# Performance work log

Hardware: AMD Instinct MI355X
Metric: run time of the kernel (lower is better)

Reference implementation:

```python
import jax, jax.numpy as jnp
import numpy as np
from jax import lax

K = 3            # kernel_size
PAD = (K - 1) // 2


def zero_insert_stride2(x):
    # tf_pad_with_stride for stride=2, f_conv!=1, padding='SAME':
    # interleave a zero BEFORE each element along W then H -> [b, 2h, 2w, c]
    b, h, w, c = x.shape
    z1 = jnp.zeros_like(x)
    med1 = jnp.stack([z1, x], axis=3).reshape(b, h, 2 * w, c)
    z2 = jnp.zeros_like(med1)
    return jnp.stack([z2, med1], axis=2).reshape(b, 2 * h, 2 * w, c)


def conv_valid(x, w):
    return lax.conv_general_dilated(
        x, w, window_strides=(1, 1), padding='VALID',
        dimension_numbers=('NHWC', 'HWIO', 'NHWC'))


def backward_conv(grad_output, inputs, kernels):
    p = PAD
    # --- grad w.r.t. input: zero-insert (stride 2), pad to FULL, conv with rot180(W)^T ---
    go = zero_insert_stride2(grad_output)                       # [B, 2h, 2w, Cout]
    fmt_inp = jnp.pad(go, ((0, 0), (p, p), (p, p), (0, 0)))     # tf_pad_to_full_conv2d (SAME)
    fmt_wt = jnp.transpose(kernels[::-1, ::-1], (0, 1, 3, 2))   # rot180 + swap I/O -> [k,k,Cout,Cin]
    grad_in = conv_valid(fmt_inp, fmt_wt)                       # [B, H, W, Cin]

    # --- grad w.r.t. weight: conv(inputs as batch-of-channels, grad_out as kernel) ---
    inp_pad = jnp.pad(inputs, ((0, 0), (p, p), (p, p), (0, 0)))  # SAME: pad inputs too
    fmt_inp2 = jnp.transpose(inp_pad, (3, 1, 2, 0))              # [Cin, H+2p, W+2p, B]
    fmt_wt2 = jnp.transpose(go, (1, 2, 0, 3))                    # NHWC->HWIO: [2h, 2w, B, Cout]
    gw = conv_valid(fmt_inp2, fmt_wt2)                           # [Cin, k, k, Cout]
    grad_wt = jnp.transpose(gw, (1, 2, 0, 3))                    # [k, k, Cin, Cout]

    # --- grad w.r.t. bias ---
    grad_bias = jnp.sum(grad_output, axis=(0, 1, 2))             # [Cout]
    return grad_in, grad_wt, grad_bias


def setup_inputs() -> dict:
    key = jax.random.key(0)
    k1, k2, k3 = jax.random.split(key, 3)
    grad_output = jax.random.normal(k1, (32, 28, 28, 256), dtype=jnp.float32)
    inputs = jax.random.normal(k2, (32, 56, 56, 256), dtype=jnp.float32)
    kernels = jax.random.normal(k3, (3, 3, 256, 256), dtype=jnp.float32)
    return {"grad_output": grad_output, "inputs": inputs, "kernels": kernels}


def reference(grad_output, inputs, kernels):
    return backward_conv(grad_output, inputs, kernels)
```

## Files before the change

### kernel.cpp

```cpp
#include <hip/hip_runtime.h>

#define Bn   32
#define HIN  56
#define WIN  56
#define Cc   256
#define HG   28
#define WG   28
#define NPIX (HG*WG)

#define GIN_SIZE (Bn*HIN*WIN*Cc)
#define GW_SIZE  (9*Cc*Cc)
#define GW_OFF   GIN_SIZE
#define BIAS_OFF (GW_OFF + GW_SIZE)

#define XT_E   (32*57*256*64)
#define GPAD_E (32*29*29*256)
#define WTB_E  (9*256*256)
#define WS_NEED ((size_t)(XT_E + GPAD_E + WTB_E) * 2)

typedef short bf16x8 __attribute__((ext_vector_type(8)));
typedef float f32x4  __attribute__((ext_vector_type(4)));

__device__ __forceinline__ unsigned short f2bf(float f) {
    return __builtin_bit_cast(unsigned short, (__bf16)f);
}

__device__ __forceinline__ void gload16(const void* g, void* lds) {
    __builtin_amdgcn_global_load_lds(
        (const __attribute__((address_space(1))) unsigned int*)g,
        (__attribute__((address_space(3))) unsigned int*)lds, 16, 0, 0);
}

__device__ __forceinline__ void full_wait_barrier() {
    asm volatile("s_waitcnt vmcnt(0) lgkmcnt(0)" ::: "memory");
    __builtin_amdgcn_s_barrier();
    __builtin_amdgcn_sched_barrier(0);
}
__device__ __forceinline__ void lgkm_wait_barrier() {
    asm volatile("s_waitcnt lgkmcnt(0)" ::: "memory");
    __builtin_amdgcn_s_barrier();
    __builtin_amdgcn_sched_barrier(0);
}
__device__ __forceinline__ void lds_barrier() {
    asm volatile("s_waitcnt lgkmcnt(0)" ::: "memory");
    __builtin_amdgcn_s_barrier();
    asm volatile("" ::: "memory");
}

__device__ __forceinline__ int swz(int row, int k) {
    int g2 = (k >> 3) ^ (row & 3) ^ ((row >> 2) & 3);
    return row * 32 + (g2 << 3) + (k & 7);
}
__device__ __forceinline__ int swz64(int row, int k) {
    int gq = ((k >> 3) ^ (row & 7) ^ ((row >> 4) & 7)) & 7;
    return row * 64 + (gq << 3) + (k & 7);
}

__global__ __launch_bounds__(256) void k_zero(float* __restrict__ p, int n) {
    int i = blockIdx.x * 256 + threadIdx.x;
    if (i < n) p[i] = 0.f;
}

__global__ __launch_bounds__(256) void k_prep_x(
    const float* __restrict__ X, unsigned short* __restrict__ xt)
{
    __shared__ unsigned short L[256 * 64];
    const int t = threadIdx.x;
    const int r = blockIdx.x;
    const int b = blockIdx.y;
    unsigned short* __restrict__ orow = xt + (size_t)((b * 57 + r) * 256) * 64;

    if (r == 56) {
        bf16x8 z = (bf16x8){0,0,0,0,0,0,0,0};
        #pragma unroll
        for (int k = 0; k < 8; ++k)
            *(bf16x8*)&orow[(size_t)(t + 256 * k) * 8] = z;
        return;
    }
    const float* __restrict__ xr = X + (size_t)((b * 56 + r) * 56) * 256;

    #pragma unroll
    for (int a = 0; a < 2; ++a) {
        const int idx = t + 256 * a;
        const int o  = idx >> 6;
        const int ci = (idx & 63) * 4;
        ushort4 ev[4], od[4];
        if (o < 7) {
            float4 xv[8];
            #pragma unroll
            for (int jj = 0; jj < 8; ++jj)
                xv[jj] = *(const float4*)(xr + (size_t)(8 * o + jj) * 256 + ci);
            #pragma unroll
            for (int c = 0; c < 4; ++c) {
                ev[c] = (ushort4){f2bf(((const float*)&xv[0])[c]), f2bf(((const float*)&xv[2])[c]),
                                  f2bf(((const float*)&xv[4])[c]), f2bf(((const float*)&xv[6])[c])};
                od[c] = (ushort4){f2bf(((const float*)&xv[1])[c]), f2bf(((const float*)&xv[3])[c]),
                                  f2bf(((const float*)&xv[5])[c]), f2bf(((const float*)&xv[7])[c])};
            }
        } else {
            #pragma unroll
            for (int c = 0; c < 4; ++c) { ev[c] = (ushort4){0,0,0,0}; od[c] = (ushort4){0,0,0,0}; }
        }
        #pragma unroll
        for (int c = 0; c < 4; ++c) {
            const int row = ci + c;
            const int rb  = (row & 7) ^ ((row >> 4) & 7);
            const int g0  = (o >> 1) ^ rb;
            const int g1  = (4 + (o >> 1)) ^ rb;
            *(ushort4*)&L[row * 64 + g0 * 8 + (o & 1) * 4] = ev[c];
            *(ushort4*)&L[row * 64 + g1 * 8 + (o & 1) * 4] = od[c];
        }
    }
    __syncthreads();
    const int rb = (t & 7) ^ ((t >> 4) & 7);
    #pragma unroll
    for (int G = 0; G < 8; ++G) {
        bf16x8 v = *(bf16x8*)&L[t * 64 + ((G ^ rb)) * 8];
        *(bf16x8*)&orow[t * 64 + G * 8] = v;
    }
}

__global__ __launch_bounds__(256) void k_prep_gpad(
    const float* __restrict__ g, unsigned short* __restrict__ gp)
{
    const int t  = threadIdx.x;
    const int iy = blockIdx.x;
    const int b  = blockIdx.y;
    const int co8 = (t & 31) * 8;
    for (int jx = (t >> 5); jx < 29; jx += 8) {
        bf16x8 v = (bf16x8){0,0,0,0,0,0,0,0};
        if (iy > 0 && jx > 0) {
            const float* src = g + (size_t)(((b * 28 + iy - 1) * 28) + jx - 1) * 256 + co8;
            float4 a0 = *(const float4*)(src);
            float4 a1 = *(const float4*)(src + 4);
            v = (bf16x8){(short)f2bf(a0.x),(short)f2bf(a0.y),(short)f2bf(a0.z),(short)f2bf(a0.w),
                         (short)f2bf(a1.x),(short)f2bf(a1.y),(short)f2bf(a1.z),(short)f2bf(a1.w)};
        }
        *(bf16x8*)&gp[(size_t)(((b * 29 + iy) * 29) + jx) * 256 + co8] = v;
    }
}

__global__ __launch_bounds__(256) void k_prep_wt(
    const float* __restrict__ w, unsigned short* __restrict__ wb)
{
    const size_t i8 = (size_t)(blockIdx.x * 256 + threadIdx.x) * 8;
    float4 a0 = *(const float4*)(w + i8);
    float4 a1 = *(const float4*)(w + i8 + 4);
    bf16x8 v = (bf16x8){(short)f2bf(a0.x),(short)f2bf(a0.y),(short)f2bf(a0.z),(short)f2bf(a0.w),
                        (short)f2bf(a1.x),(short)f2bf(a1.y),(short)f2bf(a1.z),(short)f2bf(a1.w)};
    *(bf16x8*)&wb[i8] = v;
}

__global__ __launch_bounds__(256, 2) void k_grad_in_f(
    const unsigned short* __restrict__ gpad,
    const unsigned short* __restrict__ wtb,
    float* __restrict__ out)
{
    __shared__ unsigned short At[2][128 * 64];
    __shared__ unsigned short Bt[2][128 * 64];

    const int t = threadIdx.x;
    const int l = t & 63, wave = t >> 6;
    const int mbase = (wave & 1) * 64, nbase = (wave >> 1) * 64;
    const int q = l >> 4, r16 = l & 15;
    const int mtile = blockIdx.x, ntile = blockIdx.y, cls = blockIdx.z;
    const int dy = cls >> 1, dx = cls & 1;
    const int nky = dy ? 1 : 2, nkx = dx ? 1 : 2;
    const bool nkx2 = (nkx == 2);
    const int NC = nky * nkx * 4;

    int gsv[4], ab[4], aiy[4], ajx[4];
    #pragma unroll
    for (int u = 0; u < 4; ++u) {
        const int row = u * 32 + (t >> 3);
        gsv[u] = (t & 7) ^ (row & 7) ^ ((row >> 4) & 7);
        const int P = mtile * 128 + row;
        ab[u] = P / NPIX;
        const int rem = P % NPIX;
        aiy[u] = rem / WG; ajx[u] = rem % WG;
    }

    f32x4 acc[4][4];
    #pragma unroll
    for (int a = 0; a < 4; ++a)
        #pragma unroll
        for (int b = 0; b < 4; ++b) acc[a][b] = (f32x4){0.f, 0.f, 0.f, 0.f};

    int aoff[2][4], boff[2][4];
    #pragma unroll
    for (int kk = 0; kk < 2; ++kk)
        #pragma unroll
        for (int mf = 0; mf < 4; ++mf) {
            aoff[kk][mf] = swz64(mbase + mf * 16 + r16, kk * 32 + q * 8);
            boff[kk][mf] = swz64(nbase + mf * 16 + r16, kk * 32 + q * 8);
        }

    auto prefetch = [&](int c, int buf) {
        const int tapi = c >> 2, co0 = (c & 3) << 6;
        const int ty = nkx2 ? (tapi >> 1) : tapi;
        const int tx = nkx2 ? (tapi & 1) : 0;
        const int di = dy ? 0 : (ty ? 0 : -1);
        const int dj = dx ? 0 : (tx ? 0 : -1);
        const int krow = dy ? 1 : (ty ? 0 : 2);
        const int kcol = dx ? 1 : (tx ? 0 : 2);
        const unsigned short* wb2 = wtb + (size_t)((krow * 3 + kcol) * 256 + ntile * 128) * 256 + co0;
        #pragma unroll
        for (int u = 0; u < 4; ++u) {
            const unsigned short* as2 = gpad
                + (size_t)(((ab[u] * 29 + aiy[u] + di + 1) * 29) + ajx[u] + dj + 1) * 256
                + 8 * gsv[u] + co0;
            gload16(as2, &At[buf][u * 2048 + t * 8]);
            gload16(wb2 + (size_t)(u * 32 + (t >> 3)) * 256 + 8 * gsv[u], &Bt[buf][u * 2048 + t * 8]);
        }
    };

    prefetch(0, 0);

    #pragma unroll 1
    for (int cc = 0; cc < NC; ++cc) {
        const int p = cc & 1, n = cc + 1;
        full_wait_barrier();
        if (n < NC) prefetch(n, n & 1);
        __builtin_amdgcn_sched_barrier(0);

        #pragma unroll
        for (int kk = 0; kk < 2; ++kk) {
            bf16x8 af[4], bf[4];
            #pragma unroll
            for (int mf = 0; mf < 4; ++mf) af[mf] = *(const bf16x8*)&At[p][aoff[kk][mf]];
            #pragma unroll
            for (int nf = 0; nf < 4; ++nf) bf[nf] = *(const bf16x8*)&Bt[p][boff[kk][nf]];
            #pragma unroll
            for (int mf = 0; mf < 4; ++mf)
                #pragma unroll
                for (int nf = 0; nf < 4; ++nf)
                    acc[mf][nf] = __builtin_amdgcn_mfma_f32_16x16x32_bf16(
                        af[mf], bf[nf], acc[mf][nf], 0, 0, 0);
        }
    }

    #pragma unroll
    for (int mf = 0; mf < 4; ++mf) {
        #pragma unroll
        for (int rr = 0; rr < 4; ++rr) {
            const int P   = mtile * 128 + mbase + mf * 16 + q * 4 + rr;
            const int b   = P / NPIX;
            const int rem = P % NPIX;
            const int iy  = rem / WG, jx = rem % WG;
            const int y = 2 * iy + dy, x = 2 * jx + dx;
            float* orow = out + (size_t)((b * HIN + y) * WIN + x) * Cc
                              + ntile * 128 + nbase + r16;
            #pragma unroll
            for (int nf = 0; nf < 4; ++nf) orow[nf * 16] = acc[mf][nf][rr];
        }
    }
}

__global__ __launch_bounds__(256, 3) void k_grad_wt_f(
    const unsigned short* __restrict__ xt,
    const unsigned short* __restrict__ gpad,
    float* __restrict__ gw)
{
    __shared__ unsigned short At[2][128 * 64];
    __shared__ unsigned short Bt[128 * 64];

    const int t = threadIdx.x;
    const int l = t & 63, wave = t >> 6;
    const int mbase = (wave & 1) * 64, nbase = (wave >> 1) * 64;
    const int q = l >> 4, r16 = l & 15;

    const int L   = blockIdx.x;
    const int xcd = L & 7, idx = L >> 3;
    const int b   = xcd + 8 * (idx / 36);
    const int tt  = idx % 36;
    const int tap = tt >> 2, tile = tt & 3;
    const int tci = (tile >> 1) * 128, tco = (tile & 1) * 128;
    const int ki = tap / 3, kj = tap % 3;
    const int par = (kj == 1);
    const int jsh = (kj == 2);

    const unsigned short* axp[4];
    #pragma unroll
    for (int u = 0; u < 4; ++u) {
        const int row = u * 32 + (t >> 3);
        const int gs  = (t & 7) ^ (row & 7) ^ ((row >> 4) & 7);
        const int r0  = ki + 2 * (gs >> 2);
        axp[u] = xt + (size_t)((b * 57 + r0) * 256 + tci + row) * 64 + par * 32 + (gs & 3) * 8;
    }

    const int o   = t >> 5;
    const int rs  = o >> 2;
    const int mo  = (o & 3) * 8;
    const int co4 = (t & 31) * 4;

    uint2 br[8];
    auto load_breg = [&](int cc) {
        const int i = 2 * cc + rs;
        const int base_i = (b * 29 + i + 1) * 29;
        #pragma unroll
        for (int jj = 0; jj < 8; ++jj) {
            const int j = mo + jj - jsh;
            uint2 v; v.x = 0u; v.y = 0u;
            if (j <= 27) v = *(const uint2*)(gpad + (size_t)(base_i + j + 1) * 256 + tco + co4);
            br[jj] = v;
        }
    };

    f32x4 acc[4][4];
    #pragma unroll
    for (int a = 0; a < 4; ++a)
        #pragma unroll
        for (int c = 0; c < 4; ++c) acc[a][c] = (f32x4){0.f, 0.f, 0.f, 0.f};

    int aoff[2][4], boff[2][4];
    #pragma unroll
    for (int kk = 0; kk < 2; ++kk)
        #pragma unroll
        for (int mf = 0; mf < 4; ++mf) {
            aoff[kk][mf] = swz64(mbase + mf * 16 + r16, kk * 32 + q * 8);
            boff[kk][mf] = swz64(nbase + mf * 16 + r16, kk * 32 + q * 8);
        }

    #pragma unroll
    for (int u = 0; u < 4; ++u) { gload16(axp[u], &At[0][u * 2048 + t * 8]); axp[u] += 65536; }
    load_breg(0);

    #pragma unroll 1
    for (int cc = 0; cc < 14; ++cc) {
        const int p = cc & 1, n = cc + 1;
        full_wait_barrier();
        if (n < 14) {
            #pragma unroll
            for (int u = 0; u < 4; ++u) { gload16(axp[u], &At[n & 1][u * 2048 + t * 8]); axp[u] += 65536; }
        }
        __builtin_amdgcn_sched_barrier(0);
        {
            const unsigned short* bs = (const unsigned short*)br;
            #pragma unroll
            for (int c = 0; c < 4; ++c) {
                bf16x8 wv;
                #pragma unroll
                for (int jj = 0; jj < 8; ++jj) wv[jj] = (short)bs[jj * 4 + c];
                const int row  = co4 + c;
                const int gpos = o ^ (row & 7) ^ ((row >> 4) & 7);
                *(bf16x8*)&Bt[row * 64 + gpos * 8] = wv;
            }
        }
        if (n < 14) load_breg(n);
        __builtin_amdgcn_sched_barrier(0);
        lgkm_wait_barrier();

        #pragma unroll
        for (int kk = 0; kk < 2; ++kk) {
            bf16x8 af[4], bfr[4];
            #pragma unroll
            for (int mf = 0; mf < 4; ++mf) af[mf]  = *(const bf16x8*)&At[p][aoff[kk][mf]];
            #pragma unroll
            for (int nf = 0; nf < 4; ++nf) bfr[nf] = *(const bf16x8*)&Bt[boff[kk][nf]];
            #pragma unroll
            for (int mf = 0; mf < 4; ++mf)
                #pragma unroll
                for (int nf = 0; nf < 4; ++nf)
                    acc[mf][nf] = __builtin_amdgcn_mfma_f32_16x16x32_bf16(
                        af[mf], bfr[nf], acc[mf][nf], 0, 0, 0);
        }
    }

    #pragma unroll
    for (int mf = 0; mf < 4; ++mf) {
        #pragma unroll
        for (int rr = 0; rr < 4; ++rr) {
            const int cirow = tci + mbase + mf * 16 + q * 4 + rr;
            float* dst = gw + (size_t)(tap * Cc + cirow) * Cc + tco + nbase + r16;
            #pragma unroll
            for (int nf = 0; nf < 4; ++nf) atomicAdd(dst + nf * 16, acc[mf][nf][rr]);
        }
    }
}

__global__ __launch_bounds__(256) void k_bias(
    const float* __restrict__ g, float* __restrict__ bias)
{
    const int t = threadIdx.x;
    const float* base = g + (size_t)blockIdx.x * 64 * Cc;
    float acc = 0.f;
    #pragma unroll 8
    for (int p = 0; p < 64; ++p) acc += base[(size_t)p * Cc + t];
    atomicAdd(bias + t, acc);
}

__global__ __launch_bounds__(256) void k_grad_in_fb(
    const float* __restrict__ g, const float* __restrict__ wt, float* __restrict__ out)
{
    __shared__ unsigned short ga[128 * 32];
    __shared__ unsigned short wb[128 * 32];
    const int t = threadIdx.x;
    const int l = t & 63, wave = t >> 6;
    const int mbase = (wave & 1) * 64, nbase = (wave >> 1) * 64;
    const int q = l >> 4, r16 = l & 15;
    const int mtile = blockIdx.x, ntile = blockIdx.y, cls = blockIdx.z;
    const int dy = cls >> 1, dx = cls & 1;
    const int sp = t >> 1, sc = (t & 1) * 16;
    const int P_s = mtile * 128 + sp;
    const int b_s = P_s / NPIX;
    const int rem_s = P_s % NPIX;
    const int iy_s = rem_s / WG, jx_s = rem_s % WG;
    const int sci = ntile * 128 + sp;
    f32x4 acc[4][4];
    #pragma unroll
    for (int a = 0; a < 4; ++a)
        #pragma unroll
        for (int b = 0; b < 4; ++b) acc[a][b] = (f32x4){0.f,0.f,0.f,0.f};
    int aoff[4], boff[4];
    #pragma unroll
    for (int mf = 0; mf < 4; ++mf) aoff[mf] = swz(mbase + mf * 16 + r16, q * 8);
    #pragma unroll
    for (int nf = 0; nf < 4; ++nf) boff[nf] = swz(nbase + nf * 16 + r16, q * 8);
    const int nky = dy ? 1 : 2, nkx = dx ? 1 : 2;
    for (int ty = 0; ty < nky; ++ty) {
        const int di = dy ? 0 : (ty == 0 ? -1 : 0);
        const int krow = dy ? 1 : (ty == 0 ? 2 : 0);
        for (int tx = 0; tx < nkx; ++tx) {
            const int dj = dx ? 0 : (tx == 0 ? -1 : 0);
            const int kcol = dx ? 1 : (tx == 0 ? 2 : 0);
            const int gi = iy_s + di, gj = jx_s + dj;
            const bool valid = (gi >= 0) && (gj >= 0);
            const float* __restrict__ gsrc = g + (size_t)((b_s * HG + gi) * WG + gj) * Cc + sc;
            const float* __restrict__ wsrc = wt + (size_t)((krow * 3 + kcol) * Cc + sci) * Cc + sc;
            float4 av[4], bv[4];
            #pragma unroll
            for (int u = 0; u < 4; ++u) {
                av[u] = make_float4(0.f,0.f,0.f,0.f);
                if (valid) av[u] = *(const float4*)(gsrc + u * 4);
                bv[u] = *(const float4*)(wsrc + u * 4);
            }
            #pragma unroll 1
            for (int co0 = 0; co0 < Cc; co0 += 32) {
                ushort4 ua[4], ub[4];
                #pragma unroll
                for (int u = 0; u < 4; ++u) {
                    ua[u] = (ushort4){f2bf(av[u].x), f2bf(av[u].y), f2bf(av[u].z), f2bf(av[u].w)};
                    ub[u] = (ushort4){f2bf(bv[u].x), f2bf(bv[u].y), f2bf(bv[u].z), f2bf(bv[u].w)};
                }
                if (co0 + 32 < Cc) {
                    #pragma unroll
                    for (int u = 0; u < 4; ++u) {
                        float4 a2 = make_float4(0.f,0.f,0.f,0.f);
                        if (valid) a2 = *(const float4*)(gsrc + co0 + 32 + u * 4);
                        float4 b2 = *(const float4*)(wsrc + co0 + 32 + u * 4);
                        av[u] = a2; bv[u] = b2;
                    }
                }
                lds_barrier();
                #pragma unroll
                for (int u = 0; u < 4; ++u) {
                    *(ushort4*)&ga[swz(sp, sc + u * 4)] = ua[u];
                    *(ushort4*)&wb[swz(sp, sc + u * 4)] = ub[u];
                }
                lds_barrier();
                bf16x8 af[4], bf[4];
                #pragma unroll
                for (int mf = 0; mf < 4; ++mf) af[mf] = *(const bf16x8*)&ga[aoff[mf]];
                #pragma unroll
                for (int nf = 0; nf < 4; ++nf) bf[nf] = *(const bf16x8*)&wb[boff[nf]];
                #pragma unroll
                for (int mf = 0; mf < 4; ++mf)
                    #pragma unroll
                    for (int nf = 0; nf < 4; ++nf)
                        acc[mf][nf] = __builtin_amdgcn_mfma_f32_16x16x32_bf16(
                            af[mf], bf[nf], acc[mf][nf], 0, 0, 0);
            }
        }
    }
    #pragma unroll
    for (int mf = 0; mf < 4; ++mf)
        #pragma unroll
        for (int rr = 0; rr < 4; ++rr) {
            const int P = mtile * 128 + mbase + mf * 16 + q * 4 + rr;
            const int b = P / NPIX;
            const int rem = P % NPIX;
            const int iy = rem / WG, jx = rem % WG;
            const int y = 2 * iy + dy, x = 2 * jx + dx;
            float* orow = out + (size_t)((b * HIN + y) * WIN + x) * Cc + ntile * 128 + nbase + r16;
            #pragma unroll
            for (int nf = 0; nf < 4; ++nf) orow[nf * 16] = acc[mf][nf][rr];
        }
}

__global__ __launch_bounds__(256) void k_grad_wt_fb(
    const float* __restrict__ g, const float* __restrict__ inp, float* __restrict__ gw)
{
    __shared__ unsigned short xa[128 * 64];
    __shared__ unsigned short xg[128 * 64];
    const int t = threadIdx.x;
    const int l = t & 63, wave = t >> 6;
    const int mbase = (wave & 1) * 64, nbase = (wave >> 1) * 64;
    const int q = l >> 4, r16 = l & 15;
    const int tci = (blockIdx.x >> 1) * 128, tco = (blockIdx.x & 1) * 128;
    const int tap = blockIdx.y;
    const int ki = tap / 3, kj = tap % 3;
    const int b = blockIdx.z;
    const int pg = t >> 5, p0 = pg * 8, c4 = (t & 31) * 4;
    f32x4 acc[4][4];
    #pragma unroll
    for (int a = 0; a < 4; ++a)
        #pragma unroll
        for (int c = 0; c < 4; ++c) acc[a][c] = (f32x4){0.f,0.f,0.f,0.f};
    int aoff[2][4], boff[2][4];
    #pragma unroll
    for (int kk = 0; kk < 2; ++kk)
        #pragma unroll
        for (int mf = 0; mf < 4; ++mf) {
            aoff[kk][mf] = swz64(mbase + mf * 16 + r16, kk * 32 + q * 8);
            boff[kk][mf] = swz64(nbase + mf * 16 + r16, kk * 32 + q * 8);
        }
    const float* __restrict__ gb = g + (size_t)b * NPIX * Cc;
    const float* __restrict__ ib = inp + (size_t)b * HIN * WIN * Cc;
    float4 xr[8], gr[8];
    auto load_chunk = [&](int cc) {
        #pragma unroll
        for (int j = 0; j < 8; ++j) {
            const int p = cc * 64 + p0 + j;
            const int i = p / WG, jw = p % WG;
            const int r = ki + 2 * i, s = kj + 2 * jw;
            const bool vx = (p < NPIX) && (r < HIN) && (s < WIN);
            const bool vg = (p < NPIX);
            float4 xv = make_float4(0.f,0.f,0.f,0.f), gv = xv;
            if (vx) xv = *(const float4*)(ib + (size_t)(r * WIN + s) * Cc + tci + c4);
            if (vg) gv = *(const float4*)(gb + (size_t)p * Cc + tco + c4);
            xr[j] = xv; gr[j] = gv;
        }
    };
    load_chunk(0);
    #pragma unroll 1
    for (int cc = 0; cc < 13; ++cc) {
        bf16x8 wx[4], wg[4];
        #pragma unroll
        for (int j = 0; j < 8; ++j) {
            wx[0][j] = (short)f2bf(xr[j].x); wx[1][j] = (short)f2bf(xr[j].y);
            wx[2][j] = (short)f2bf(xr[j].z); wx[3][j] = (short)f2bf(xr[j].w);
            wg[0][j] = (short)f2bf(gr[j].x); wg[1][j] = (short)f2bf(gr[j].y);
            wg[2][j] = (short)f2bf(gr[j].z); wg[3][j] = (short)f2bf(gr[j].w);
        }
        if (cc + 1 < 13) load_chunk(cc + 1);
        lds_barrier();
        #pragma unroll
        for (int c = 0; c < 4; ++c) {
            *(bf16x8*)&xa[swz64(c4 + c, p0)] = wx[c];
            *(bf16x8*)&xg[swz64(c4 + c, p0)] = wg[c];
        }
        lds_barrier();
        #pragma unroll
        for (int kk = 0; kk < 2; ++kk) {
            bf16x8 af[4], bfr[4];
            #pragma unroll
            for (int mf = 0; mf < 4; ++mf) af[mf] = *(const bf16x8*)&xa[aoff[kk][mf]];
            #pragma unroll
            for (int nf = 0; nf < 4; ++nf) bfr[nf] = *(const bf16x8*)&xg[boff[kk][nf]];
            #pragma unroll
            for (int mf = 0; mf < 4; ++mf)
                #pragma unroll
                for (int nf = 0; nf < 4; ++nf)
                    acc[mf][nf] = __builtin_amdgcn_mfma_f32_16x16x32_bf16(
                        af[mf], bfr[nf], acc[mf][nf], 0, 0, 0);
        }
    }
    #pragma unroll
    for (int mf = 0; mf < 4; ++mf)
        #pragma unroll
        for (int rr = 0; rr < 4; ++rr) {
            const int cirow = tci + mbase + mf * 16 + q * 4 + rr;
            float* dst = gw + (size_t)(tap * Cc + cirow) * Cc + tco + nbase + r16;
            #pragma unroll
            for (int nf = 0; nf < 4; ++nf) atomicAdd(dst + nf * 16, acc[mf][nf][rr]);
        }
}

extern "C" void kernel_launch(void* const* d_in, const int* in_sizes, int n_in,
                              void* d_out, int out_size, void* d_ws, size_t ws_size,
                              hipStream_t stream) {
    const float* g   = (const float*)d_in[0];
    const float* inp = (const float*)d_in[1];
    const float* wt  = (const float*)d_in[2];
    float* out = (float*)d_out;

    const int nzero = GW_SIZE + 256;
    k_zero<<<(nzero + 255) / 256, 256, 0, stream>>>(out + GW_OFF, nzero);

    if (ws_size >= WS_NEED) {
        unsigned short* xt  = (unsigned short*)d_ws;
        unsigned short* gp  = xt + XT_E;
        unsigned short* wtb = gp + GPAD_E;
        k_prep_x   <<<dim3(57, 32), 256, 0, stream>>>(inp, xt);
        k_prep_gpad<<<dim3(29, 32), 256, 0, stream>>>(g, gp);
        k_prep_wt  <<<WTB_E / 2048, 256, 0, stream>>>(wt, wtb);
        k_grad_in_f<<<dim3(196, 2, 4), 256, 0, stream>>>(gp, wtb, out);
        k_grad_wt_f<<<1152, 256, 0, stream>>>(xt, gp, out + GW_OFF);
    } else {
        k_grad_in_fb<<<dim3(196, 2, 4), 256, 0, stream>>>(g, wt, out);
        k_grad_wt_fb<<<dim3(4, 9, 32), 256, 0, stream>>>(g, inp, out + GW_OFF);
    }
    k_bias<<<392, 256, 0, stream>>>(g, out + BIAS_OFF);
}
```

Measured before the change: 203.2 us.

## Double-buffer B tile in grad-weight kernel and compute bias from bf16 padded grads

```diff
diff --git a/kernel.cpp b/kernel.cpp
--- a/kernel.cpp
+++ b/kernel.cpp
@@ -24,6 +24,10 @@
 __device__ __forceinline__ unsigned short f2bf(float f) {
     return __builtin_bit_cast(unsigned short, (__bf16)f);
 }
+__device__ __forceinline__ float bf2f(unsigned short u) {
+    union { unsigned int u; float f; } v; v.u = ((unsigned int)u) << 16;
+    return v.f;
+}
 
 __device__ __forceinline__ void gload16(const void* g, void* lds) {
     __builtin_amdgcn_global_load_lds(
@@ -33,11 +37,6 @@
 
 __device__ __forceinline__ void full_wait_barrier() {
     asm volatile("s_waitcnt vmcnt(0) lgkmcnt(0)" ::: "memory");
-    __builtin_amdgcn_s_barrier();
-    __builtin_amdgcn_sched_barrier(0);
-}
-__device__ __forceinline__ void lgkm_wait_barrier() {
-    asm volatile("s_waitcnt lgkmcnt(0)" ::: "memory");
     __builtin_amdgcn_s_barrier();
     __builtin_amdgcn_sched_barrier(0);
 }
@@ -256,13 +255,13 @@
     }
 }
 
-__global__ __launch_bounds__(256, 3) void k_grad_wt_f(
+__global__ __launch_bounds__(256, 2) void k_grad_wt_f(
     const unsigned short* __restrict__ xt,
     const unsigned short* __restrict__ gpad,
     float* __restrict__ gw)
 {
     __shared__ unsigned short At[2][128 * 64];
-    __shared__ unsigned short Bt[128 * 64];
+    __shared__ unsigned short Bt[2][128 * 64];
 
     const int t = threadIdx.x;
     const int l = t & 63, wave = t >> 6;
@@ -305,6 +304,18 @@
             br[jj] = v;
         }
     };
+    auto repack_b = [&](int buf) {
+        const unsigned short* bs = (const unsigned short*)br;
+        #pragma unroll
+        for (int c = 0; c < 4; ++c) {
+            bf16x8 wv;
+            #pragma unroll
+            for (int jj = 0; jj < 8; ++jj) wv[jj] = (short)bs[jj * 4 + c];
+            const int row  = co4 + c;
+            const int gpos = o ^ (row & 7) ^ ((row >> 4) & 7);
+            *(bf16x8*)&Bt[buf][row * 64 + gpos * 8] = wv;
+        }
+    };
 
     f32x4 acc[4][4];
     #pragma unroll
@@ -324,6 +335,9 @@
     #pragma unroll
     for (int u = 0; u < 4; ++u) { gload16(axp[u], &At[0][u * 2048 + t * 8]); axp[u] += 65536; }
     load_breg(0);
+    asm volatile("s_waitcnt vmcnt(0)" ::: "memory");
+    repack_b(0);
+    load_breg(1);
 
     #pragma unroll 1
     for (int cc = 0; cc < 14; ++cc) {
@@ -332,23 +346,10 @@
         if (n < 14) {
             #pragma unroll
             for (int u = 0; u < 4; ++u) { gload16(axp[u], &At[n & 1][u * 2048 + t * 8]); axp[u] += 65536; }
+            repack_b(n & 1);
+            if (n + 1 < 14) load_breg(n + 1);
         }
         __builtin_amdgcn_sched_barrier(0);
-        {
-            const unsigned short* bs = (const unsigned short*)br;
-            #pragma unroll
-            for (int c = 0; c < 4; ++c) {
-                bf16x8 wv;
-                #pragma unroll
-                for (int jj = 0; jj < 8; ++jj) wv[jj] = (short)bs[jj * 4 + c];
-                const int row  = co4 + c;
-                const int gpos = o ^ (row & 7) ^ ((row >> 4) & 7);
-                *(bf16x8*)&Bt[row * 64 + gpos * 8] = wv;
-            }
-        }
-        if (n < 14) load_breg(n);
-        __builtin_amdgcn_sched_barrier(0);
-        lgkm_wait_barrier();
 
         #pragma unroll
         for (int kk = 0; kk < 2; ++kk) {
@@ -356,7 +357,7 @@
             #pragma unroll
             for (int mf = 0; mf < 4; ++mf) af[mf]  = *(const bf16x8*)&At[p][aoff[kk][mf]];
             #pragma unroll
-            for (int nf = 0; nf < 4; ++nf) bfr[nf] = *(const bf16x8*)&Bt[boff[kk][nf]];
+            for (int nf = 0; nf < 4; ++nf) bfr[nf] = *(const bf16x8*)&Bt[p][boff[kk][nf]];
             #pragma unroll
             for (int mf = 0; mf < 4; ++mf)
                 #pragma unroll
@@ -376,6 +377,20 @@
             for (int nf = 0; nf < 4; ++nf) atomicAdd(dst + nf * 16, acc[mf][nf][rr]);
         }
     }
+}
+
+__global__ __launch_bounds__(256) void k_bias_gp(
+    const unsigned short* __restrict__ gp, float* __restrict__ bias)
+{
+    const int t = threadIdx.x;
+    const int row0 = blockIdx.x * 64;
+    float acc = 0.f;
+    #pragma unroll 8
+    for (int p = 0; p < 64; ++p) {
+        const int row = row0 + p;
+        if (row < 32 * 29 * 29) acc += bf2f(gp[(size_t)row * Cc + t]);
+    }
+    atomicAdd(bias + t, acc);
 }
 
 __global__ __launch_bounds__(256) void k_bias(
@@ -596,9 +611,10 @@
         k_prep_wt  <<<WTB_E / 2048, 256, 0, stream>>>(wt, wtb);
         k_grad_in_f<<<dim3(196, 2, 4), 256, 0, stream>>>(gp, wtb, out);
         k_grad_wt_f<<<1152, 256, 0, stream>>>(xt, gp, out + GW_OFF);
+        k_bias_gp  <<<421, 256, 0, stream>>>(gp, out + BIAS_OFF);
     } else {
         k_grad_in_fb<<<dim3(196, 2, 4), 256, 0, stream>>>(g, wt, out);
         k_grad_wt_fb<<<dim3(4, 9, 32), 256, 0, stream>>>(g, inp, out + GW_OFF);
-    }
-    k_bias<<<392, 256, 0, stream>>>(g, out + BIAS_OFF);
-}
+        k_bias<<<392, 256, 0, stream>>>(g, out + BIAS_OFF);
+    }
+}
```

New measurement: 229.3 us. +12.8%, slower.

## Fuse kj=0 and kj=2 weight-gradient taps into one block sharing A tiles

Applied to the files above, without the earlier changes.

```diff
diff --git a/kernel.cpp b/kernel.cpp
--- a/kernel.cpp
+++ b/kernel.cpp
@@ -256,13 +256,14 @@
     }
 }
 
-__global__ __launch_bounds__(256, 3) void k_grad_wt_f(
+__global__ __launch_bounds__(256, 2) void k_grad_wt_f(
     const unsigned short* __restrict__ xt,
     const unsigned short* __restrict__ gpad,
     float* __restrict__ gw)
 {
     __shared__ unsigned short At[2][128 * 64];
-    __shared__ unsigned short Bt[128 * 64];
+    __shared__ unsigned short Bt0[128 * 64];
+    __shared__ unsigned short Bt2[128 * 64];
 
     const int t = threadIdx.x;
     const int l = t & 63, wave = t >> 6;
@@ -271,13 +272,13 @@
 
     const int L   = blockIdx.x;
     const int xcd = L & 7, idx = L >> 3;
-    const int b   = xcd + 8 * (idx / 36);
-    const int tt  = idx % 36;
-    const int tap = tt >> 2, tile = tt & 3;
+    const bool heavy = idx < 48;
+    const int hid = heavy ? idx : idx - 48;
+    const int b   = xcd + 8 * (hid / 12);
+    const int tt  = hid % 12;
+    const int ki  = tt >> 2, tile = tt & 3;
     const int tci = (tile >> 1) * 128, tco = (tile & 1) * 128;
-    const int ki = tap / 3, kj = tap % 3;
-    const int par = (kj == 1);
-    const int jsh = (kj == 2);
+    const int par = heavy ? 0 : 1;
 
     const unsigned short* axp[4];
     #pragma unroll
@@ -293,24 +294,32 @@
     const int mo  = (o & 3) * 8;
     const int co4 = (t & 31) * 4;
 
-    uint2 br[8];
+    uint2 br[8], brm1;
     auto load_breg = [&](int cc) {
         const int i = 2 * cc + rs;
         const int base_i = (b * 29 + i + 1) * 29;
         #pragma unroll
         for (int jj = 0; jj < 8; ++jj) {
-            const int j = mo + jj - jsh;
+            const int j = mo + jj;
             uint2 v; v.x = 0u; v.y = 0u;
             if (j <= 27) v = *(const uint2*)(gpad + (size_t)(base_i + j + 1) * 256 + tco + co4);
             br[jj] = v;
         }
+        if (heavy) {
+            uint2 v; v.x = 0u; v.y = 0u;
+            if (mo > 0) v = *(const uint2*)(gpad + (size_t)(base_i + mo) * 256 + tco + co4);
+            brm1 = v;
+        }
     };
 
-    f32x4 acc[4][4];
+    f32x4 acc0[4][4], acc2[4][4];
     #pragma unroll
     for (int a = 0; a < 4; ++a)
         #pragma unroll
-        for (int c = 0; c < 4; ++c) acc[a][c] = (f32x4){0.f, 0.f, 0.f, 0.f};
+        for (int c = 0; c < 4; ++c) {
+            acc0[a][c] = (f32x4){0.f, 0.f, 0.f, 0.f};
+            acc2[a][c] = (f32x4){0.f, 0.f, 0.f, 0.f};
+        }
 
     int aoff[2][4], boff[2][4];
     #pragma unroll
@@ -335,15 +344,23 @@
         }
         __builtin_amdgcn_sched_barrier(0);
         {
-            const unsigned short* bs = (const unsigned short*)br;
+            const unsigned short* bs  = (const unsigned short*)br;
+            const unsigned short* bm1 = (const unsigned short*)&brm1;
             #pragma unroll
             for (int c = 0; c < 4; ++c) {
-                bf16x8 wv;
-                #pragma unroll
-                for (int jj = 0; jj < 8; ++jj) wv[jj] = (short)bs[jj * 4 + c];
                 const int row  = co4 + c;
                 const int gpos = o ^ (row & 7) ^ ((row >> 4) & 7);
-                *(bf16x8*)&Bt[row * 64 + gpos * 8] = wv;
+                bf16x8 wv;
+                #pragma unroll
+                for (int jj = 0; jj < 8; ++jj) wv[jj] = (short)bs[jj * 4 + c];
+                *(bf16x8*)&Bt0[row * 64 + gpos * 8] = wv;
+                if (heavy) {
+                    bf16x8 w2;
+                    w2[0] = (short)bm1[c];
+                    #pragma unroll
+                    for (int jj = 1; jj < 8; ++jj) w2[jj] = (short)bs[(jj - 1) * 4 + c];
+                    *(bf16x8*)&Bt2[row * 64 + gpos * 8] = w2;
+                }
             }
         }
         if (n < 14) load_breg(n);
@@ -352,28 +369,53 @@
 
         #pragma unroll
         for (int kk = 0; kk < 2; ++kk) {
-            bf16x8 af[4], bfr[4];
+            bf16x8 af[4], bf0[4];
             #pragma unroll
             for (int mf = 0; mf < 4; ++mf) af[mf]  = *(const bf16x8*)&At[p][aoff[kk][mf]];
             #pragma unroll
-            for (int nf = 0; nf < 4; ++nf) bfr[nf] = *(const bf16x8*)&Bt[boff[kk][nf]];
+            for (int nf = 0; nf < 4; ++nf) bf0[nf] = *(const bf16x8*)&Bt0[boff[kk][nf]];
             #pragma unroll
             for (int mf = 0; mf < 4; ++mf)
                 #pragma unroll
                 for (int nf = 0; nf < 4; ++nf)
-                    acc[mf][nf] = __builtin_amdgcn_mfma_f32_16x16x32_bf16(
-                        af[mf], bfr[nf], acc[mf][nf], 0, 0, 0);
-        }
-    }
-
+                    acc0[mf][nf] = __builtin_amdgcn_mfma_f32_16x16x32_bf16(
+                        af[mf], bf0[nf], acc0[mf][nf], 0, 0, 0);
+            if (heavy) {
+                bf16x8 bf2[4];
+                #pragma unroll
+                for (int nf = 0; nf < 4; ++nf) bf2[nf] = *(const bf16x8*)&Bt2[boff[kk][nf]];
+                #pragma unroll
+                for (int mf = 0; mf < 4; ++mf)
+                    #pragma unroll
+                    for (int nf = 0; nf < 4; ++nf)
+                        acc2[mf][nf] = __builtin_amdgcn_mfma_f32_16x16x32_bf16(
+                            af[mf], bf2[nf], acc2[mf][nf], 0, 0, 0);
+            }
+        }
+    }
+
+    const int tap0 = heavy ? (ki * 3 + 0) : (ki * 3 + 1);
     #pragma unroll
     for (int mf = 0; mf < 4; ++mf) {
         #pragma unroll
         for (int rr = 0; rr < 4; ++rr) {
             const int cirow = tci + mbase + mf * 16 + q * 4 + rr;
-            float* dst = gw + (size_t)(tap * Cc + cirow) * Cc + tco + nbase + r16;
-            #pragma unroll
-            for (int nf = 0; nf < 4; ++nf) atomicAdd(dst + nf * 16, acc[mf][nf][rr]);
+            float* dst = gw + (size_t)(tap0 * Cc + cirow) * Cc + tco + nbase + r16;
+            #pragma unroll
+            for (int nf = 0; nf < 4; ++nf) atomicAdd(dst + nf * 16, acc0[mf][nf][rr]);
+        }
+    }
+    if (heavy) {
+        const int tap2 = ki * 3 + 2;
+        #pragma unroll
+        for (int mf = 0; mf < 4; ++mf) {
+            #pragma unroll
+            for (int rr = 0; rr < 4; ++rr) {
+                const int cirow = tci + mbase + mf * 16 + q * 4 + rr;
+                float* dst = gw + (size_t)(tap2 * Cc + cirow) * Cc + tco + nbase + r16;
+                #pragma unroll
+                for (int nf = 0; nf < 4; ++nf) atomicAdd(dst + nf * 16, acc2[mf][nf][rr]);
+            }
         }
     }
 }
@@ -595,7 +637,7 @@
         k_prep_gpad<<<dim3(29, 32), 256, 0, stream>>>(g, gp);
         k_prep_wt  <<<WTB_E / 2048, 256, 0, stream>>>(wt, wtb);
         k_grad_in_f<<<dim3(196, 2, 4), 256, 0, stream>>>(gp, wtb, out);
-        k_grad_wt_f<<<1152, 256, 0, stream>>>(xt, gp, out + GW_OFF);
+        k_grad_wt_f<<<768, 256, 0, stream>>>(xt, gp, out + GW_OFF);
     } else {
         k_grad_in_fb<<<dim3(196, 2, 4), 256, 0, stream>>>(g, wt, out);
         k_grad_wt_fb<<<dim3(4, 9, 32), 256, 0, stream>>>(g, inp, out + GW_OFF);
```

Result: slower. 210.4 us (+3.5%).
